# Performance work log

Hardware: AMD Instinct MI355X
Metric: run time of the kernel (lower is better)

## Reference

```python
import jax, jax.numpy as jnp
import numpy as np

N, M, K = 32768, 16, 64
HALF_LOG_2PI = 0.9189385332046727  # 0.5*log(2*pi)
EPS = 2.220446049250313e-16       # np.finfo(np.float64).eps, as in original


def setup_inputs() -> dict:
    key = jax.random.key(0)
    k1, k2, k3 = jax.random.split(key, 3)
    X = jax.random.normal(k1, (N, M), dtype=jnp.float32)
    wk0_logits = jnp.ones((1, K), dtype=jnp.float32)
    W_logits = jnp.ones((M, K, K), dtype=jnp.float32)
    mu = jax.random.uniform(k2, (M, K, K), dtype=jnp.float32, minval=-4.0, maxval=4.0)
    pre_sigma = jax.random.uniform(k3, (M, K, K), dtype=jnp.float32, minval=0.0, maxval=5.0)
    return {"X": X, "wk0_logits": wk0_logits, "W_logits": W_logits,
            "mu": mu, "pre_sigma": pre_sigma}


def reference(X, wk0_logits, W_logits, mu, pre_sigma):
    n, k = X.shape[0], wk0_logits.shape[1]
    wk0 = jax.nn.softmax(wk0_logits, axis=1)[0]          # (K,)
    # tf softmax(W_logits[i], axis=0) == softmax over axis=1 of (M,K,K)
    logW = jax.nn.log_softmax(W_logits, axis=1)          # (M,K,K)
    sigma = jax.nn.softplus(pre_sigma)                   # (M,K,K)

    prod0 = jnp.broadcast_to(jnp.eye(k, dtype=X.dtype), (n, k, k))

    def step(prod, inputs):
        x, lw, m, s = inputs                             # x:(N,), lw/m/s:(K,K)
        # Normal(mu, sigma).log_prob(x)
        z = (x[:, None, None] - m) / s                   # (N,K,K)
        logp = -0.5 * jnp.square(z) - jnp.log(s) - HALF_LOG_2PI
        result = jnp.exp(lw + logp)                      # (N,K,K)
        # prod @ result^T per sample
        new_prod = jnp.einsum('nij,nkj->nik', prod, result)
        return new_prod, None

    prod, _ = jax.lax.scan(step, prod0, (X.T, logW, mu, sigma))
    # squeeze(wk0 @ prod) summed over last axis -> (N,)
    likelihoods = jnp.einsum('k,nkj->n', wk0, prod)
    return jnp.log(likelihoods + EPS)
```

## Files before the change

kernel.cpp:

```cpp
#include <hip/hip_runtime.h>
#include <math.h>


#define TTG_N 32768
#define TTG_M 16
#define TTG_K 64

typedef float f32x2 __attribute__((ext_vector_type(2)));
typedef float f32x4 __attribute__((ext_vector_type(4)));

static constexpr float kHalfLog2Pi = 0.9189385332046727f;
static constexpr float kEps        = 2.220446049250313e-16f;
static constexpr float kLog2e      = 1.4426950408889634f;

#if defined(__has_builtin)
#if __has_builtin(__builtin_amdgcn_exp2f)
#define TTG_EXP2(x) __builtin_amdgcn_exp2f(x)
#else
#define TTG_EXP2(x) exp2f(x)
#endif
#else
#define TTG_EXP2(x) exp2f(x)
#endif

#define PKFMA(d, a, b, c) \
  asm("v_pk_fma_f32 %0, %1, %2, %3" : "=v"(d) : "v"(a), "v"(b), "v"(c))

__global__ void ttg_prep_wk0(const float* __restrict__ logits,
                             float* __restrict__ wk0) {
  int i = threadIdx.x;
  float l = logits[i];
  float mx = l;
  for (int d = 1; d < 64; d <<= 1) mx = fmaxf(mx, __shfl_xor(mx, d));
  float e = expf(l - mx);
  float s = e;
  for (int d = 1; d < 64; d <<= 1) s += __shfl_xor(s, d);
  wk0[i] = e / s;
}

__global__ void ttg_prep_params(const float* __restrict__ W,
                                const float* __restrict__ mu,
                                const float* __restrict__ ps,
                                float* __restrict__ P) {
  int b = blockIdx.x;
  int m = b >> 6;
  int j = b & 63;
  int i = threadIdx.x;
  int idx = (m * TTG_K + i) * TTG_K + j;

  float w = W[idx];
  float mx = w;
  for (int d = 1; d < 64; d <<= 1) mx = fmaxf(mx, __shfl_xor(mx, d));
  float e = expf(w - mx);
  float s = e;
  for (int d = 1; d < 64; d <<= 1) s += __shfl_xor(s, d);
  float lw = w - mx - logf(s);

  float mv  = mu[idx];
  float sig = log1pf(expf(ps[idx]));
  float inv2 = 1.0f / (sig * sig);
  float A = -0.5f * inv2 * kLog2e;
  float B = mv * inv2 * kLog2e;
  float C = (lw - logf(sig) - kHalfLog2Pi - 0.5f * mv * mv * inv2) * kLog2e;

  float* base = P + (size_t)m * 12288;
  int pi = ((j >> 2) * TTG_K + i) * 4 + (j & 3);
  base[pi]        = A;
  base[4096 + pi] = B;
  base[8192 + pi] = C;
}

__global__ __launch_bounds__(1024, 4) void ttg_main(
    const float* __restrict__ X, const float* __restrict__ P,
    const float* __restrict__ wk0, float* __restrict__ out) {
  __shared__ __align__(16) float prA[TTG_K * TTG_K];
  __shared__ __align__(16) float prB[TTG_K * TTG_K];
  __shared__ __align__(16) float prC[TTG_K * TTG_K];
  __shared__ __align__(16) float ub[64 * TTG_K];
  __shared__ __align__(16) float xbT[TTG_M * 64];

  const int tid  = threadIdx.x;
  const int lane = tid & 63;
  const int wv   = __builtin_amdgcn_readfirstlane(tid >> 6);
  const int blk  = blockIdx.x;

  if (tid < 256) {
    float4 v = ((const float4*)X)[blk * 256 + tid];
    int s = tid >> 2, f0 = (tid & 3) * 4;
    xbT[(f0 + 0) * 64 + s] = v.x;
    xbT[(f0 + 1) * 64 + s] = v.y;
    xbT[(f0 + 2) * 64 + s] = v.z;
    xbT[(f0 + 3) * 64 + s] = v.w;
  }
#pragma unroll
  for (int r = 0; r < 4; ++r) {
    int idx = tid + r * 1024;
    ub[idx] = wk0[idx & 63];
  }
  {
    const float4* src = (const float4*)P;
    ((float4*)prA)[tid] = src[tid];
    ((float4*)prB)[tid] = src[1024 + tid];
    ((float4*)prC)[tid] = src[2048 + tid];
  }
  __syncthreads();

  float aA0, aB0, aA1, aB1, aA2, aB2, aA3, aB3;
  for (int m = 0; m < TTG_M; ++m) {
    const float* xr = xbT + m * 64 + wv * 4;
    const f32x2 xs0 = {xr[0], xr[0]};
    const f32x2 xs1 = {xr[1], xr[1]};
    const f32x2 xs2 = {xr[2], xr[2]};
    const f32x2 xs3 = {xr[3], xr[3]};

    aA0 = aB0 = aA1 = aB1 = aA2 = aB2 = aA3 = aB3 = 0.f;
    const f32x4* pA = ((const f32x4*)prA) + lane;
    const f32x4* pB = ((const f32x4*)prB) + lane;
    const f32x4* pC = ((const f32x4*)prC) + lane;
    const f32x4* pU = (const f32x4*)(ub + wv * 4 * TTG_K);

#define TTG_S(S, XS, AA, AB)                                                  \
    {                                                                         \
      const f32x4 u4 = pU[(S) * 16 + j4];                 \
      f32x2 h0, h1, tlo, thi;                                                 \
      PKFMA(h0, alo, XS, blo);                                                \
      PKFMA(tlo, h0, XS, clo);                                                \
      PKFMA(h1, ahi, XS, bhi);                                                \
      PKFMA(thi, h1, XS, chi);                                                \
      AA = fmaf(TTG_EXP2(tlo[0]), u4.x, AA);                                  \
      AB = fmaf(TTG_EXP2(tlo[1]), u4.y, AB);                                  \
      AA = fmaf(TTG_EXP2(thi[0]), u4.z, AA);                                  \
      AB = fmaf(TTG_EXP2(thi[1]), u4.w, AB);                                  \
    }

#pragma unroll
    for (int j4 = 0; j4 < 16; ++j4) {
      const f32x4 a4 = pA[j4 * 64];
      const f32x4 b4 = pB[j4 * 64];
      const f32x4 c4 = pC[j4 * 64];
      const f32x2 alo = __builtin_shufflevector(a4, a4, 0, 1);
      const f32x2 ahi = __builtin_shufflevector(a4, a4, 2, 3);
      const f32x2 blo = __builtin_shufflevector(b4, b4, 0, 1);
      const f32x2 bhi = __builtin_shufflevector(b4, b4, 2, 3);
      const f32x2 clo = __builtin_shufflevector(c4, c4, 0, 1);
      const f32x2 chi = __builtin_shufflevector(c4, c4, 2, 3);
      TTG_S(0, xs0, aA0, aB0)
      TTG_S(1, xs1, aA1, aB1)
      TTG_S(2, xs2, aA2, aB2)
      TTG_S(3, xs3, aA3, aB3)
    }
#undef TTG_S

    if (m < TTG_M - 1) {
      __syncthreads();
      float* ud = ub + wv * 4 * TTG_K + lane;
      ud[0 * TTG_K] = aA0 + aB0;
      ud[1 * TTG_K] = aA1 + aB1;
      ud[2 * TTG_K] = aA2 + aB2;
      ud[3 * TTG_K] = aA3 + aB3;
      const float4* src = (const float4*)(P + (size_t)(m + 1) * 12288);
      float4 pf0 = src[tid];
      float4 pf1 = src[tid + 1024];
      float4 pf2 = src[tid + 2048];
      ((float4*)prA)[tid] = pf0;
      ((float4*)prB)[tid] = pf1;
      ((float4*)prC)[tid] = pf2;
      __syncthreads();
    }
  }

  float r[4] = {aA0 + aB0, aA1 + aB1, aA2 + aB2, aA3 + aB3};
#pragma unroll
  for (int c = 0; c < 4; ++c) {
#pragma unroll
    for (int d = 1; d < 64; d <<= 1) r[c] += __shfl_xor(r[c], d);
  }
  if (lane == 0) {
    const int s0 = blk * 64 + wv * 4;
#pragma unroll
    for (int c = 0; c < 4; ++c) out[s0 + c] = logf(r[c] + kEps);
  }
}

extern "C" void kernel_launch(void* const* d_in, const int* in_sizes, int n_in,
                              void* d_out, int out_size, void* d_ws, size_t ws_size,
                              hipStream_t stream) {
  const float* X   = (const float*)d_in[0];
  const float* wl  = (const float*)d_in[1];
  const float* W   = (const float*)d_in[2];
  const float* mu  = (const float*)d_in[3];
  const float* ps  = (const float*)d_in[4];
  float* out = (float*)d_out;

  float* wk0 = (float*)d_ws;
  float* P   = wk0 + 256;

  ttg_prep_wk0<<<1, 64, 0, stream>>>(wl, wk0);
  ttg_prep_params<<<TTG_M * TTG_K, 64, 0, stream>>>(W, mu, ps, P);
  ttg_main<<<TTG_N / 64, 1024, 0, stream>>>(X, P, wk0, out);
}
```

Baseline: 260.5 us.

## Prefetch next step's params into registers before compute; drop packed FMA path

The global loads of the next step's A/B/C parameters now happen at the start of each step, so their latency overlaps the exp/FMA work instead of sitting between the two barriers. The inline-asm packed FMA evaluation is replaced by scalar FMAs that use a precomputed x^2 and a single accumulator per sample. The added cost is 12 extra live registers across the compute loop, which may pressure occupancy under the 1024x4 launch bounds. Scalar FMAs also give up the packed-math throughput of v_pk_fma_f32, and the single accumulator per sample lengthens the dependency chain.

```diff
diff --git a/kernel.cpp b/kernel.cpp
--- a/kernel.cpp
+++ b/kernel.cpp
@@ -6,7 +6,6 @@
 #define TTG_M 16
 #define TTG_K 64
 
-typedef float f32x2 __attribute__((ext_vector_type(2)));
 typedef float f32x4 __attribute__((ext_vector_type(4)));
 
 static constexpr float kHalfLog2Pi = 0.9189385332046727f;
@@ -22,9 +21,6 @@
 #else
 #define TTG_EXP2(x) exp2f(x)
 #endif
-
-#define PKFMA(d, a, b, c) \
-  asm("v_pk_fma_f32 %0, %1, %2, %3" : "=v"(d) : "v"(a), "v"(b), "v"(c))
 
 __global__ void ttg_prep_wk0(const float* __restrict__ logits,
                              float* __restrict__ wk0) {
@@ -105,63 +101,55 @@
   }
   __syncthreads();
 
-  float aA0, aB0, aA1, aB1, aA2, aB2, aA3, aB3;
+  float acc0, acc1, acc2, acc3;
   for (int m = 0; m < TTG_M; ++m) {
+    float4 pf0, pf1, pf2;
+    if (m < TTG_M - 1) {
+      const float4* src = (const float4*)(P + (size_t)(m + 1) * 12288);
+      pf0 = src[tid];
+      pf1 = src[tid + 1024];
+      pf2 = src[tid + 2048];
+    }
     const float* xr = xbT + m * 64 + wv * 4;
-    const f32x2 xs0 = {xr[0], xr[0]};
-    const f32x2 xs1 = {xr[1], xr[1]};
-    const f32x2 xs2 = {xr[2], xr[2]};
-    const f32x2 xs3 = {xr[3], xr[3]};
+    const float x0 = xr[0], x1 = xr[1], x2 = xr[2], x3 = xr[3];
+    const float y0 = x0 * x0, y1 = x1 * x1, y2 = x2 * x2, y3 = x3 * x3;
 
-    aA0 = aB0 = aA1 = aB1 = aA2 = aB2 = aA3 = aB3 = 0.f;
+    acc0 = acc1 = acc2 = acc3 = 0.f;
     const f32x4* pA = ((const f32x4*)prA) + lane;
     const f32x4* pB = ((const f32x4*)prB) + lane;
     const f32x4* pC = ((const f32x4*)prC) + lane;
     const f32x4* pU = (const f32x4*)(ub + wv * 4 * TTG_K);
-
-#define TTG_S(S, XS, AA, AB)                                                  \
-    {                                                                         \
-      const f32x4 u4 = pU[(S) * 16 + j4];                 \
-      f32x2 h0, h1, tlo, thi;                                                 \
-      PKFMA(h0, alo, XS, blo);                                                \
-      PKFMA(tlo, h0, XS, clo);                                                \
-      PKFMA(h1, ahi, XS, bhi);                                                \
-      PKFMA(thi, h1, XS, chi);                                                \
-      AA = fmaf(TTG_EXP2(tlo[0]), u4.x, AA);                                  \
-      AB = fmaf(TTG_EXP2(tlo[1]), u4.y, AB);                                  \
-      AA = fmaf(TTG_EXP2(thi[0]), u4.z, AA);                                  \
-      AB = fmaf(TTG_EXP2(thi[1]), u4.w, AB);                                  \
-    }
 
 #pragma unroll
     for (int j4 = 0; j4 < 16; ++j4) {
       const f32x4 a4 = pA[j4 * 64];
       const f32x4 b4 = pB[j4 * 64];
       const f32x4 c4 = pC[j4 * 64];
-      const f32x2 alo = __builtin_shufflevector(a4, a4, 0, 1);
-      const f32x2 ahi = __builtin_shufflevector(a4, a4, 2, 3);
-      const f32x2 blo = __builtin_shufflevector(b4, b4, 0, 1);
-      const f32x2 bhi = __builtin_shufflevector(b4, b4, 2, 3);
-      const f32x2 clo = __builtin_shufflevector(c4, c4, 0, 1);
-      const f32x2 chi = __builtin_shufflevector(c4, c4, 2, 3);
-      TTG_S(0, xs0, aA0, aB0)
-      TTG_S(1, xs1, aA1, aB1)
-      TTG_S(2, xs2, aA2, aB2)
-      TTG_S(3, xs3, aA3, aB3)
+      const f32x4 u0q = pU[j4];
+      const f32x4 u1q = pU[16 + j4];
+      const f32x4 u2q = pU[32 + j4];
+      const f32x4 u3q = pU[48 + j4];
+#pragma unroll
+      for (int q = 0; q < 4; ++q) {
+        const float a = a4[q], b = b4[q], c = c4[q];
+        float t0 = fmaf(a, y0, fmaf(b, x0, c));
+        float t1 = fmaf(a, y1, fmaf(b, x1, c));
+        float t2 = fmaf(a, y2, fmaf(b, x2, c));
+        float t3 = fmaf(a, y3, fmaf(b, x3, c));
+        acc0 = fmaf(TTG_EXP2(t0), u0q[q], acc0);
+        acc1 = fmaf(TTG_EXP2(t1), u1q[q], acc1);
+        acc2 = fmaf(TTG_EXP2(t2), u2q[q], acc2);
+        acc3 = fmaf(TTG_EXP2(t3), u3q[q], acc3);
+      }
     }
-#undef TTG_S
 
     if (m < TTG_M - 1) {
       __syncthreads();
       float* ud = ub + wv * 4 * TTG_K + lane;
-      ud[0 * TTG_K] = aA0 + aB0;
-      ud[1 * TTG_K] = aA1 + aB1;
-      ud[2 * TTG_K] = aA2 + aB2;
-      ud[3 * TTG_K] = aA3 + aB3;
-      const float4* src = (const float4*)(P + (size_t)(m + 1) * 12288);
-      float4 pf0 = src[tid];
-      float4 pf1 = src[tid + 1024];
-      float4 pf2 = src[tid + 2048];
+      ud[0 * TTG_K] = acc0;
+      ud[1 * TTG_K] = acc1;
+      ud[2 * TTG_K] = acc2;
+      ud[3 * TTG_K] = acc3;
       ((float4*)prA)[tid] = pf0;
       ((float4*)prB)[tid] = pf1;
       ((float4*)prC)[tid] = pf2;
@@ -169,7 +157,7 @@
     }
   }
 
-  float r[4] = {aA0 + aB0, aA1 + aB1, aA2 + aB2, aA3 + aB3};
+  float r[4] = {acc0, acc1, acc2, acc3};
 #pragma unroll
   for (int c = 0; c < 4; ++c) {
 #pragma unroll
```

After: 306.4 us. 17.6% more time.
